# Optimization experiments

Measured on AMD Instinct MI355X. Metric: run time of the kernel, lower is better.

Reference implementation:

```python
import jax, jax.numpy as jnp
import numpy as np

POOL = (2, 2, 2)   # LPPool3d kernel == stride
KH, KW = 3, 3      # unfold kernel
EPS = 1e-6


def setup_inputs() -> dict:
    key = jax.random.key(0)
    k1, k2, k3 = jax.random.split(key, 3)
    x = jax.random.normal(k1, (32, 8, 4, 256, 256), dtype=jnp.float32)
    patch_dim = 8 * (4 // POOL[0]) * KH * KW  # 144
    out_dim = 128
    lin_w = jax.random.normal(k2, (out_dim, patch_dim), dtype=jnp.float32) * (1.0 / np.sqrt(patch_dim))
    lin_b = jax.random.normal(k3, (out_dim,), dtype=jnp.float32) * 0.01
    return {"x": x, "lin_w": lin_w, "lin_b": lin_b}


def reference(x, lin_w, lin_b):
    N, C, D, H, W = x.shape
    kd, kh, kw = POOL
    # LPPool3d with p=2, stride==kernel: (sum of squares in window)^(1/2)
    xr = (x * x).reshape(N, C, D // kd, kd, H // kh, kh, W // kw, kw)
    pooled = jnp.sqrt(xr.sum(axis=(3, 5, 7)))  # (N, C, Dp, Hp, Wp)
    Dp, Hp, Wp = pooled.shape[2], pooled.shape[3], pooled.shape[4]
    # merge depth into channels: permute(0,2,1,3,4).view(N, Dp*C, Hp, Wp)
    merged = pooled.transpose(0, 2, 1, 3, 4).reshape(N, Dp * C, Hp, Wp)
    MC = Dp * C
    Ho, Wo = Hp - KH + 1, Wp - KW + 1
    # im2col matching torch.nn.Unfold ordering: (channel, kh, kw) flattened
    slices = [merged[:, :, i:i + Ho, j:j + Wo] for i in range(KH) for j in range(KW)]
    patches = jnp.stack(slices, axis=2)                 # (N, MC, KH*KW, Ho, Wo)
    patches = patches.reshape(N, MC * KH * KW, Ho * Wo) # (N, patch_dim, L)
    patches = patches.transpose(0, 2, 1)                # (N, L, patch_dim)
    # per-patch linear + CELU (alpha=1)
    proj = jnp.einsum('nlk,ok->nlo', patches, lin_w) + lin_b  # (N, L, out_dim)
    act = jax.nn.celu(proj)
    # aggregate over patches, then L2-normalize with clamped norm
    agg = act.mean(axis=1)                              # (N, out_dim)
    norm = jnp.maximum(jnp.linalg.norm(agg, axis=1, keepdims=True), EPS)
    return agg / norm
```

## Files before the change

kernel.cpp:

```cpp
#include <hip/hip_runtime.h>
#include <math.h>

#define NB   32
#define C    8
#define D    4
#define H    256
#define W    256
#define HP   128
#define WP   128
#define MC   16
#define HO   126
#define WO   126
#define PATCH 144
#define OUTD 128
#define NL   (HO*WO)
#define HOG  6
#define NGRP (HO/HOG)
#define PROWS 9
#define BROW 168
#define NPOOLB 2048

typedef float  f32x4  __attribute__((ext_vector_type(4)));
typedef __bf16 bf16x8 __attribute__((ext_vector_type(8)));

__global__ __launch_bounds__(256, 4)
void pool_kernel(const float* __restrict__ x, const float* __restrict__ lin_w,
                 __bf16* __restrict__ Pg, __bf16* __restrict__ Bw) {
    int t = threadIdx.x;
    int b = blockIdx.x;

    if (b == NPOOLB) {
        int o = t & 127, kh = t >> 7;
#pragma unroll 4
        for (int kk = 0; kk < 80; kk++) {
            int kn = kh*80 + kk;
            int tap = kn >> 4, mc = kn & 15;
            float v = (tap < 9) ? lin_w[o*PATCH + mc*9 + tap] : 0.f;
            Bw[o*BROW + kn] = (__bf16)v;
        }
        return;
    }

    int wp2 = t & 63;
    int dph = (t >> 6) & 1;
    int g = b*2 + (t >> 7);
    int hp = g & 127, n = g >> 7;

    const float* xn = x + (size_t)n * (C*D*H*W) + (size_t)(2*dph) * (H*W)
                        + (2*hp)*W + 4*wp2;
    bf16x8 pk0, pk1;
#pragma unroll 2
    for (int c = 0; c < 8; c++) {
        const float* xb = xn + (size_t)c * (D*H*W);
        f32x4 a0 = *(const f32x4*)(xb);
        f32x4 a1 = *(const f32x4*)(xb + W);
        f32x4 a2 = *(const f32x4*)(xb + H*W);
        f32x4 a3 = *(const f32x4*)(xb + H*W + W);
        float s0 = a0.x*a0.x + a0.y*a0.y + a1.x*a1.x + a1.y*a1.y
                 + a2.x*a2.x + a2.y*a2.y + a3.x*a3.x + a3.y*a3.y;
        float s1 = a0.z*a0.z + a0.w*a0.w + a1.z*a1.z + a1.w*a1.w
                 + a2.z*a2.z + a2.w*a2.w + a3.z*a3.z + a3.w*a3.w;
        pk0[c] = (__bf16)sqrtf(s0);
        pk1[c] = (__bf16)sqrtf(s1);
    }
    __bf16* pr = Pg + ((size_t)n*HP + hp) * (WP*MC);
    *(bf16x8*)&pr[(2*wp2    )*16 + dph*8] = pk0;
    *(bf16x8*)&pr[(2*wp2 + 1)*16 + dph*8] = pk1;
}

__global__ __launch_bounds__(256, 2)
void gemm_kernel(const __bf16* __restrict__ Pg, const __bf16* __restrict__ Bw,
                 const float* __restrict__ lin_b, float* __restrict__ accg) {
    __shared__ __align__(16) char smem[PROWS*128*32 + OUTD*BROW*2];
    __bf16* Pl   = (__bf16*)smem;
    __bf16* Blds = (__bf16*)(smem + PROWS*128*32);

    int blk = blockIdx.x;
    int g = blk % NGRP, n = blk / NGRP;
    int ho0 = g * HOG;
    int t = threadIdx.x;
    int wave = t >> 6, lane = t & 63, quad = lane >> 4, l16 = lane & 15;

    {
        const f32x4* src = (const f32x4*)(Pg + ((size_t)n*HP + ho0) * (WP*MC));
        f32x4* dst = (f32x4*)Pl;
#pragma unroll
        for (int r = 0; r < 8; r++) dst[r*256 + t] = src[r*256 + t];
        f32x4 z = {};
        dst[8*256 + t] = z;
        const f32x4* bsrc = (const f32x4*)Bw;
        f32x4* bdst = (f32x4*)Blds;
#pragma unroll
        for (int r = 0; r < 10; r++) bdst[r*256 + t] = bsrc[r*256 + t];
        if (t < 128) bdst[10*256 + t] = bsrc[10*256 + t];
    }

    float lb[8];
#pragma unroll
    for (int nt = 0; nt < 8; nt++) lb[nt] = lin_b[nt*16 + l16];

    __syncthreads();

    float srun[8] = {0,0,0,0,0,0,0,0};
    int h8 = (quad & 1) * 8;
    int m0 = wave * 32 + l16;

    for (int hp = 0; hp < HOG/2; hp++) {
        f32x4 acc[2][2][8] = {};
#pragma unroll
        for (int ks = 0; ks < 5; ks++) {
            int tap = 2*ks + (quad >> 1);
            int it = (tap * 11) >> 5;
            int jt = tap - it * 3;
            bf16x8 bfr[8];
#pragma unroll
            for (int nt = 0; nt < 8; nt++)
                bfr[nt] = *(const bf16x8*)&Blds[(nt*16 + l16)*BROW + ks*32 + quad*8];
            bf16x8 afr[2][2];
#pragma unroll
            for (int h = 0; h < 2; h++)
#pragma unroll
                for (int mt = 0; mt < 2; mt++) {
                    int m = m0 + mt*16;
                    afr[h][mt] = *(const bf16x8*)&Pl[((hp*2 + h + it)*128 + m + jt)*16 + h8];
                }
#pragma unroll
            for (int nt = 0; nt < 8; nt++) {
                acc[0][0][nt] = __builtin_amdgcn_mfma_f32_16x16x32_bf16(afr[0][0], bfr[nt], acc[0][0][nt], 0, 0, 0);
                acc[0][1][nt] = __builtin_amdgcn_mfma_f32_16x16x32_bf16(afr[0][1], bfr[nt], acc[0][1][nt], 0, 0, 0);
                acc[1][0][nt] = __builtin_amdgcn_mfma_f32_16x16x32_bf16(afr[1][0], bfr[nt], acc[1][0][nt], 0, 0, 0);
                acc[1][1][nt] = __builtin_amdgcn_mfma_f32_16x16x32_bf16(afr[1][1], bfr[nt], acc[1][1][nt], 0, 0, 0);
            }
        }
#pragma unroll
        for (int h = 0; h < 2; h++) {
#pragma unroll
            for (int nt = 0; nt < 8; nt++) {
                float s = 0.f;
#pragma unroll
                for (int mt = 0; mt < 2; mt++) {
                    int mb = wave*32 + mt*16 + quad*4;
#pragma unroll
                    for (int r = 0; r < 4; r++) {
                        float p = acc[h][mt][nt][r] + lb[nt];
                        float a = (p > 0.f) ? p : (__expf(p) - 1.f);
                        if (mb + r < WO) s += a;
                    }
                }
                s += __shfl_xor(s, 16, 64);
                s += __shfl_xor(s, 32, 64);
                srun[nt] += s;
            }
        }
    }

    __syncthreads();
    float* red = (float*)smem;
    if (quad == 0) {
#pragma unroll
        for (int nt = 0; nt < 8; nt++) red[wave*OUTD + nt*16 + l16] = srun[nt];
    }
    __syncthreads();
    if (t < OUTD) {
        float tot = red[t] + red[OUTD+t] + red[2*OUTD+t] + red[3*OUTD+t];
        atomicAdd(&accg[n*OUTD + t], tot);
    }
}

__global__ __launch_bounds__(256, 2)
void fused_kernel(const float* __restrict__ x, const float* __restrict__ lin_w,
                  const float* __restrict__ lin_b, float* __restrict__ accg) {
    __shared__ __align__(16) char smem[PROWS*128*32 + OUTD*BROW*2];
    __bf16* Pl   = (__bf16*)smem;
    __bf16* Blds = (__bf16*)(smem + PROWS*128*32);

    int blk = blockIdx.x;
    int g = blk % NGRP, n = blk / NGRP;
    int ho0 = g * HOG;
    int t = threadIdx.x;
    int wave = t >> 6, lane = t & 63, quad = lane >> 4, l16 = lane & 15;

    {
        int wp = t & 127, dph = t >> 7;
        const float* xn = x + (size_t)n * (C*D*H*W);
#pragma unroll 2
        for (int i = 0; i < 8; i++) {
            int hp = ho0 + i;
            bf16x8 pk;
#pragma unroll
            for (int c = 0; c < 8; c++) {
                const float* xb = xn + ((c*4 + 2*dph) * H + 2*hp) * W + 2*wp;
                float2 a0 = *(const float2*)(xb);
                float2 a1 = *(const float2*)(xb + W);
                float2 a2 = *(const float2*)(xb + H*W);
                float2 a3 = *(const float2*)(xb + H*W + W);
                float s = a0.x*a0.x + a0.y*a0.y + a1.x*a1.x + a1.y*a1.y
                        + a2.x*a2.x + a2.y*a2.y + a3.x*a3.x + a3.y*a3.y;
                pk[c] = (__bf16)sqrtf(s);
            }
            *(bf16x8*)&Pl[(i*128 + wp)*16 + dph*8] = pk;
        }
        bf16x8 z = {};
        *(bf16x8*)&Pl[(8*128 + wp)*16 + dph*8] = z;
    }
    {
        int o = t & 127, kh = t >> 7;
#pragma unroll 4
        for (int kk = 0; kk < 80; kk++) {
            int kn = kh*80 + kk;
            int tap = kn >> 4, mc = kn & 15;
            float v = (tap < 9) ? lin_w[o*PATCH + mc*9 + tap] : 0.f;
            Blds[o*BROW + kn] = (__bf16)v;
        }
    }

    float lb[8];
#pragma unroll
    for (int nt = 0; nt < 8; nt++) lb[nt] = lin_b[nt*16 + l16];

    __syncthreads();

    float srun[8] = {0,0,0,0,0,0,0,0};
    int h8 = (quad & 1) * 8;
    int m0 = wave * 32 + l16;

    for (int hh = 0; hh < HOG; hh++) {
        f32x4 acc[2][8] = {};
#pragma unroll
        for (int ks = 0; ks < 5; ks++) {
            int tap = 2*ks + (quad >> 1);
            int it = (tap * 11) >> 5;
            int jt = tap - it * 3;
            bf16x8 afr[2];
#pragma unroll
            for (int mt = 0; mt < 2; mt++) {
                int m = m0 + mt*16;
                afr[mt] = *(const bf16x8*)&Pl[((hh + it)*128 + m + jt)*16 + h8];
            }
#pragma unroll
            for (int nt = 0; nt < 8; nt++) {
                bf16x8 bfr = *(const bf16x8*)&Blds[(nt*16 + l16)*BROW + ks*32 + quad*8];
                acc[0][nt] = __builtin_amdgcn_mfma_f32_16x16x32_bf16(afr[0], bfr, acc[0][nt], 0, 0, 0);
                acc[1][nt] = __builtin_amdgcn_mfma_f32_16x16x32_bf16(afr[1], bfr, acc[1][nt], 0, 0, 0);
            }
        }
#pragma unroll
        for (int nt = 0; nt < 8; nt++) {
            float s = 0.f;
#pragma unroll
            for (int mt = 0; mt < 2; mt++) {
                int mb = wave*32 + mt*16 + quad*4;
#pragma unroll
                for (int r = 0; r < 4; r++) {
                    float p = acc[mt][nt][r] + lb[nt];
                    float a = (p > 0.f) ? p : (__expf(p) - 1.f);
                    if (mb + r < WO) s += a;
                }
            }
            s += __shfl_xor(s, 16, 64);
            s += __shfl_xor(s, 32, 64);
            srun[nt] += s;
        }
    }

    __syncthreads();
    float* red = (float*)smem;
    if (quad == 0) {
#pragma unroll
        for (int nt = 0; nt < 8; nt++) red[wave*OUTD + nt*16 + l16] = srun[nt];
    }
    __syncthreads();
    if (t < OUTD) {
        float tot = red[t] + red[OUTD+t] + red[2*OUTD+t] + red[3*OUTD+t];
        atomicAdd(&accg[n*OUTD + t], tot);
    }
}

__global__ void finalize_kernel(const float* __restrict__ acc, float* __restrict__ out) {
    int n = blockIdx.x;
    int o = threadIdx.x;
    float a = acc[n * OUTD + o] * (1.0f / (float)NL);
    float s = a * a;
#pragma unroll
    for (int off = 32; off > 0; off >>= 1) s += __shfl_down(s, off, 64);
    __shared__ float partial[2];
    if ((o & 63) == 0) partial[o >> 6] = s;
    __syncthreads();
    float norm = sqrtf(partial[0] + partial[1]);
    norm = fmaxf(norm, 1e-6f);
    out[n * OUTD + o] = a / norm;
}

extern "C" void kernel_launch(void* const* d_in, const int* in_sizes, int n_in,
                              void* d_out, int out_size, void* d_ws, size_t ws_size,
                              hipStream_t stream) {
    const float* x     = (const float*)d_in[0];
    const float* lin_w = (const float*)d_in[1];
    const float* lin_b = (const float*)d_in[2];
    float* out = (float*)d_out;

    float* acc = (float*)d_ws;
    hipMemsetAsync(acc, 0, NB * OUTD * sizeof(float), stream);

    const size_t BW_BYTES = (size_t)OUTD * BROW * sizeof(__bf16);
    const size_t PG_BYTES = (size_t)NB * HP * WP * MC * sizeof(__bf16);
    if (ws_size >= 16384 + BW_BYTES + PG_BYTES) {
        __bf16* Bw = (__bf16*)((char*)d_ws + 16384);
        __bf16* Pg = (__bf16*)((char*)d_ws + 16384 + BW_BYTES);
        pool_kernel<<<NPOOLB + 1, 256, 0, stream>>>(x, lin_w, Pg, Bw);
        gemm_kernel<<<NB * NGRP, 256, 0, stream>>>(Pg, Bw, lin_b, acc);
    } else {
        fused_kernel<<<NB * NGRP, 256, 0, stream>>>(x, lin_w, lin_b, acc);
    }
    finalize_kernel<<<NB, OUTD, 0, stream>>>(acc, out);
}
```

Measured before the change: 462.3 us.

## Split GEMM block into 8 waves with three output rows each

```diff
diff --git a/kernel.cpp b/kernel.cpp
--- a/kernel.cpp
+++ b/kernel.cpp
@@ -68,7 +68,7 @@
     *(bf16x8*)&pr[(2*wp2 + 1)*16 + dph*8] = pk1;
 }
 
-__global__ __launch_bounds__(256, 2)
+__global__ __launch_bounds__(512, 4)
 void gemm_kernel(const __bf16* __restrict__ Pg, const __bf16* __restrict__ Bw,
                  const float* __restrict__ lin_b, float* __restrict__ accg) {
     __shared__ __align__(16) char smem[PROWS*128*32 + OUTD*BROW*2];
@@ -80,19 +80,20 @@
     int ho0 = g * HOG;
     int t = threadIdx.x;
     int wave = t >> 6, lane = t & 63, quad = lane >> 4, l16 = lane & 15;
+    int wr = wave & 3, h0 = (wave >> 2) * 3;
 
     {
         const f32x4* src = (const f32x4*)(Pg + ((size_t)n*HP + ho0) * (WP*MC));
         f32x4* dst = (f32x4*)Pl;
 #pragma unroll
-        for (int r = 0; r < 8; r++) dst[r*256 + t] = src[r*256 + t];
+        for (int r = 0; r < 4; r++) dst[r*512 + t] = src[r*512 + t];
         f32x4 z = {};
-        dst[8*256 + t] = z;
+        if (t < 256) dst[2048 + t] = z;
         const f32x4* bsrc = (const f32x4*)Bw;
         f32x4* bdst = (f32x4*)Blds;
 #pragma unroll
-        for (int r = 0; r < 10; r++) bdst[r*256 + t] = bsrc[r*256 + t];
-        if (t < 128) bdst[10*256 + t] = bsrc[10*256 + t];
+        for (int r = 0; r < 5; r++) bdst[r*512 + t] = bsrc[r*512 + t];
+        if (t < 128) bdst[2560 + t] = bsrc[2560 + t];
     }
 
     float lb[8];
@@ -103,54 +104,44 @@
 
     float srun[8] = {0,0,0,0,0,0,0,0};
     int h8 = (quad & 1) * 8;
-    int m0 = wave * 32 + l16;
-
-    for (int hp = 0; hp < HOG/2; hp++) {
-        f32x4 acc[2][2][8] = {};
+    int m0 = wr * 32 + l16;
+
+    for (int hh = h0; hh < h0 + 3; hh++) {
+        f32x4 acc[2][8] = {};
 #pragma unroll
         for (int ks = 0; ks < 5; ks++) {
             int tap = 2*ks + (quad >> 1);
             int it = (tap * 11) >> 5;
             int jt = tap - it * 3;
-            bf16x8 bfr[8];
-#pragma unroll
-            for (int nt = 0; nt < 8; nt++)
-                bfr[nt] = *(const bf16x8*)&Blds[(nt*16 + l16)*BROW + ks*32 + quad*8];
-            bf16x8 afr[2][2];
-#pragma unroll
-            for (int h = 0; h < 2; h++)
-#pragma unroll
-                for (int mt = 0; mt < 2; mt++) {
-                    int m = m0 + mt*16;
-                    afr[h][mt] = *(const bf16x8*)&Pl[((hp*2 + h + it)*128 + m + jt)*16 + h8];
+            bf16x8 afr[2];
+#pragma unroll
+            for (int mt = 0; mt < 2; mt++) {
+                int m = m0 + mt*16;
+                afr[mt] = *(const bf16x8*)&Pl[((hh + it)*128 + m + jt)*16 + h8];
+            }
+#pragma unroll
+            for (int nt = 0; nt < 8; nt++) {
+                bf16x8 bfr = *(const bf16x8*)&Blds[(nt*16 + l16)*BROW + ks*32 + quad*8];
+                acc[0][nt] = __builtin_amdgcn_mfma_f32_16x16x32_bf16(afr[0], bfr, acc[0][nt], 0, 0, 0);
+                acc[1][nt] = __builtin_amdgcn_mfma_f32_16x16x32_bf16(afr[1], bfr, acc[1][nt], 0, 0, 0);
+            }
+        }
+#pragma unroll
+        for (int nt = 0; nt < 8; nt++) {
+            float s = 0.f;
+#pragma unroll
+            for (int mt = 0; mt < 2; mt++) {
+                int mb = wr*32 + mt*16 + quad*4;
+#pragma unroll
+                for (int r = 0; r < 4; r++) {
+                    float p = acc[mt][nt][r] + lb[nt];
+                    float a = (p > 0.f) ? p : (__expf(p) - 1.f);
+                    if (mb + r < WO) s += a;
                 }
-#pragma unroll
-            for (int nt = 0; nt < 8; nt++) {
-                acc[0][0][nt] = __builtin_amdgcn_mfma_f32_16x16x32_bf16(afr[0][0], bfr[nt], acc[0][0][nt], 0, 0, 0);
-                acc[0][1][nt] = __builtin_amdgcn_mfma_f32_16x16x32_bf16(afr[0][1], bfr[nt], acc[0][1][nt], 0, 0, 0);
-                acc[1][0][nt] = __builtin_amdgcn_mfma_f32_16x16x32_bf16(afr[1][0], bfr[nt], acc[1][0][nt], 0, 0, 0);
-                acc[1][1][nt] = __builtin_amdgcn_mfma_f32_16x16x32_bf16(afr[1][1], bfr[nt], acc[1][1][nt], 0, 0, 0);
-            }
-        }
-#pragma unroll
-        for (int h = 0; h < 2; h++) {
-#pragma unroll
-            for (int nt = 0; nt < 8; nt++) {
-                float s = 0.f;
-#pragma unroll
-                for (int mt = 0; mt < 2; mt++) {
-                    int mb = wave*32 + mt*16 + quad*4;
-#pragma unroll
-                    for (int r = 0; r < 4; r++) {
-                        float p = acc[h][mt][nt][r] + lb[nt];
-                        float a = (p > 0.f) ? p : (__expf(p) - 1.f);
-                        if (mb + r < WO) s += a;
-                    }
-                }
-                s += __shfl_xor(s, 16, 64);
-                s += __shfl_xor(s, 32, 64);
-                srun[nt] += s;
-            }
+            }
+            s += __shfl_xor(s, 16, 64);
+            s += __shfl_xor(s, 32, 64);
+            srun[nt] += s;
         }
     }
 
@@ -162,7 +153,9 @@
     }
     __syncthreads();
     if (t < OUTD) {
-        float tot = red[t] + red[OUTD+t] + red[2*OUTD+t] + red[3*OUTD+t];
+        float tot = 0.f;
+#pragma unroll
+        for (int w = 0; w < 8; w++) tot += red[w*OUTD + t];
         atomicAdd(&accg[n*OUTD + t], tot);
     }
 }
@@ -308,7 +301,7 @@
         __bf16* Bw = (__bf16*)((char*)d_ws + 16384);
         __bf16* Pg = (__bf16*)((char*)d_ws + 16384 + BW_BYTES);
         pool_kernel<<<NPOOLB + 1, 256, 0, stream>>>(x, lin_w, Pg, Bw);
-        gemm_kernel<<<NB * NGRP, 256, 0, stream>>>(Pg, Bw, lin_b, acc);
+        gemm_kernel<<<NB * NGRP, 512, 0, stream>>>(Pg, Bw, lin_b, acc);
     } else {
         fused_kernel<<<NB * NGRP, 256, 0, stream>>>(x, lin_w, lin_b, acc);
     }
```

Measured after the change: 537.4 us. +16.2%, slower.
